# Optimization experiments

Measured on AMD Instinct MI355X. Metric: run time of the kernel, lower is better.

## Reference

```python
import jax, jax.numpy as jnp
import numpy as np

B, C, H, W = 8, 128, 128, 128
D_MODEL = C
D_INNER = 2 * D_MODEL          # expand=2 -> 256
D_STATE = 64
HEADDIM = 32                   # _resolve_headdim(128, 32) -> 32
NHEADS = D_INNER // HEADDIM    # 8
D_CONV = 4
CHUNK = 64
GN_GROUPS = 8                  # _group_count(128, 8)
D_XBC = D_INNER + 2 * D_STATE  # 384
D_INPROJ = 2 * D_INNER + 2 * D_STATE + NHEADS  # 648


def _group_norm(x, g, b, groups=GN_GROUPS, eps=1e-5):
    Bn, Cn, Hh, Ww = x.shape
    xr = x.reshape(Bn, groups, Cn // groups, Hh, Ww)
    mu = xr.mean(axis=(2, 3, 4), keepdims=True)
    var = xr.var(axis=(2, 3, 4), keepdims=True)
    xr = (xr - mu) * jax.lax.rsqrt(var + eps)
    return xr.reshape(Bn, Cn, Hh, Ww) * g[None, :, None, None] + b[None, :, None, None]


def _grid_sample_bilinear_border(img, grid):
    # img: (B,C,H,W); grid: (B,H,W,2) with (x,y) in [-1,1]; align_corners=True, border padding
    _, _, Hh, Ww = img.shape
    gx = jnp.clip((grid[..., 0] + 1.0) * 0.5 * (Ww - 1), 0.0, Ww - 1.0)
    gy = jnp.clip((grid[..., 1] + 1.0) * 0.5 * (Hh - 1), 0.0, Hh - 1.0)
    x0 = jnp.floor(gx); y0 = jnp.floor(gy)
    wx = gx - x0; wy = gy - y0
    x0i = x0.astype(jnp.int32); y0i = y0.astype(jnp.int32)
    x1i = jnp.minimum(x0i + 1, Ww - 1); y1i = jnp.minimum(y0i + 1, Hh - 1)
    def per_b(im, y0b, y1b, x0b, x1b, wxb, wyb):
        v00 = im[:, y0b, x0b]; v01 = im[:, y0b, x1b]
        v10 = im[:, y1b, x0b]; v11 = im[:, y1b, x1b]
        return (v00 * (1 - wxb) + v01 * wxb) * (1 - wyb) + (v10 * (1 - wxb) + v11 * wxb) * wyb
    return jax.vmap(per_b)(img, y0i, y1i, x0i, x1i, wx, wy)


def _mamba(seq, in_proj_w, conv_w, conv_b, dt_bias, A_log, D_skip, norm_g, out_w):
    # seq: (Bs, L, d_model) -> (Bs, L, d_model); Mamba2/SSD-style selective scan
    Bs, L, _ = seq.shape
    pad = (CHUNK - L % CHUNK) % CHUNK
    if pad:
        seq = jnp.pad(seq, ((0, 0), (0, pad), (0, 0)))
    Lp = L + pad
    zxbcdt = jnp.einsum('bld,ed->ble', seq, in_proj_w)
    z = zxbcdt[..., :D_INNER]
    xBC = zxbcdt[..., D_INNER:D_INNER + D_XBC]
    dt = jax.nn.softplus(zxbcdt[..., -NHEADS:] + dt_bias)  # (Bs,Lp,nh)
    # causal depthwise conv1d, kernel D_CONV
    xp = jnp.pad(xBC, ((0, 0), (D_CONV - 1, 0), (0, 0)))
    xBC = sum(conv_w[:, k] * xp[:, k:k + Lp, :] for k in range(D_CONV)) + conv_b
    xBC = jax.nn.silu(xBC)
    xs = xBC[..., :D_INNER].reshape(Bs, Lp, NHEADS, HEADDIM)
    Bm = xBC[..., D_INNER:D_INNER + D_STATE]
    Cm = xBC[..., D_INNER + D_STATE:]
    A = -jnp.exp(A_log)  # (nh,)
    def step(h, inp):
        x_t, B_t, C_t, dt_t = inp  # (Bs,nh,hd),(Bs,ds),(Bs,ds),(Bs,nh)
        dA = jnp.exp(dt_t * A)  # (Bs,nh)
        h = h * dA[..., None, None] + (dt_t[..., None] * x_t)[..., None] * B_t[:, None, None, :]
        y = jnp.einsum('bhds,bs->bhd', h, C_t)
        return h, y
    h0 = jnp.zeros((Bs, NHEADS, HEADDIM, D_STATE), seq.dtype)
    _, ys = jax.lax.scan(step, h0, (jnp.moveaxis(xs, 1, 0), jnp.moveaxis(Bm, 1, 0), jnp.moveaxis(Cm, 1, 0), jnp.moveaxis(dt, 1, 0)))
    ys = jnp.moveaxis(ys, 0, 1) + D_skip[None, None, :, None] * xs  # (Bs,Lp,nh,hd)
    y = ys.reshape(Bs, Lp, D_INNER) * jax.nn.silu(z)  # gated
    y = y * jax.lax.rsqrt(jnp.mean(y * y, axis=-1, keepdims=True) + 1e-5) * norm_g  # RMSNorm
    out = jnp.einsum('ble,de->bld', y, out_w)
    return out[:, :L] if pad else out


def _forward(x, dw_w, gn_g, gn_b, pw_w, pw_b, in_proj_w, conv_w, conv_b, dt_bias, A_log, D_skip, norm_g, out_w):
    Bn, Cn, Hh, Ww = x.shape
    dn = ('NCHW', 'OIHW', 'NCHW')
    # offset_net: depthwise 5x5 -> GroupNorm -> GELU -> 1x1
    h1 = jax.lax.conv_general_dilated(x, dw_w, (1, 1), 'SAME', feature_group_count=Cn, dimension_numbers=dn)
    h1 = jax.nn.gelu(_group_norm(h1, gn_g, gn_b), approximate=False)
    off = jax.lax.conv_general_dilated(h1, pw_w, (1, 1), 'SAME', dimension_numbers=dn) + pw_b[None, :, None, None]
    offset = jnp.tanh(off) * min(8.0, max(Hh, Ww) * 0.1)  # (B,1,H,W)
    gy = jnp.linspace(-1.0, 1.0, Hh, dtype=x.dtype)
    gx = jnp.linspace(-1.0, 1.0, Ww, dtype=x.dtype)
    base_y, base_x = jnp.meshgrid(gy, gx, indexing='ij')  # (H,W)
    off_n = offset[:, 0] * (2.0 / max(Hh - 1, 1))  # horizontal scan: vertical offsets
    grid = jnp.stack([jnp.broadcast_to(base_x, (Bn, Hh, Ww)), jnp.clip(base_y + off_n, -1.0, 1.0)], axis=-1)
    deformed = _grid_sample_bilinear_border(x, grid)
    seq = deformed.transpose(0, 2, 3, 1).reshape(Bn * Hh, Ww, Cn)  # (b h) w c
    out = _mamba(seq, in_proj_w, conv_w, conv_b, dt_bias, A_log, D_skip, norm_g, out_w)
    out_2d = out.reshape(Bn, Hh, Ww, Cn).transpose(0, 3, 1, 2)
    return out_2d, offset


def setup_inputs() -> dict:
    key = jax.random.key(0)
    ks = jax.random.split(key, 8)
    return {
        'x': jax.random.normal(ks[0], (B, C, H, W), jnp.float32),
        'dw_w': jax.random.normal(ks[1], (C, 1, 5, 5), jnp.float32) * 0.05,
        'gn_g': jnp.ones((C,), jnp.float32),
        'gn_b': jnp.zeros((C,), jnp.float32),
        'pw_w': jax.random.normal(ks[2], (1, C, 1, 1), jnp.float32) * 0.02,
        'pw_b': jnp.zeros((1,), jnp.float32),
        'in_proj_w': jax.random.normal(ks[3], (D_INPROJ, D_MODEL), jnp.float32) * 0.02,
        'conv_w': jax.random.normal(ks[4], (D_XBC, D_CONV), jnp.float32) * 0.1,
        'conv_b': jnp.zeros((D_XBC,), jnp.float32),
        'dt_bias': jax.random.normal(ks[5], (NHEADS,), jnp.float32) * 0.1,
        'A_log': jnp.log(jnp.arange(1, NHEADS + 1, dtype=jnp.float32)),
        'D_skip': jnp.ones((NHEADS,), jnp.float32),
        'norm_g': jnp.ones((D_INNER,), jnp.float32),
        'out_w': jax.random.normal(ks[6], (D_MODEL, D_INNER), jnp.float32) * 0.02,
    }


def reference(x, dw_w, gn_g, gn_b, pw_w, pw_b, in_proj_w, conv_w, conv_b, dt_bias, A_log, D_skip, norm_g, out_w):
    return _forward(x, dw_w, gn_g, gn_b, pw_w, pw_b, in_proj_w, conv_w, conv_b, dt_bias, A_log, D_skip, norm_g, out_w)
```

## Files before the change

kernel.cpp:

```cpp
#include <hip/hip_runtime.h>
#include <math.h>


typedef _Float16 half8 __attribute__((ext_vector_type(8)));
typedef _Float16 half4 __attribute__((ext_vector_type(4)));
typedef float f32x4 __attribute__((ext_vector_type(4)));

__device__ __forceinline__ float b2f(unsigned short u) {
  return __uint_as_float(((unsigned int)u) << 16);
}
__device__ __forceinline__ bool in_is_f32(const void* gng) {
  return ((const unsigned int*)gng)[0] == 0x3F800000u;
}

#define P_DWW 0
#define P_CW 3200
#define P_CB 4736
#define P_GNG 5120
#define P_GNB 5248
#define P_PWW 5376
#define P_PWB 5504
#define P_DTB 5505
#define P_ALOG 5513
#define P_DSKIP 5521
#define P_NG 5529

__global__ void k_prep_params(const void* dww, const void* cw, const void* cb,
                              const void* gng, const void* gnb, const void* pww,
                              const void* pwb, const void* dtbias, const void* alog,
                              const void* dskip, const void* ng, float* __restrict__ P,
                              float* __restrict__ gst) {
  bool f = in_is_f32(gng);
  int tid = threadIdx.x;
  if (tid < 128) gst[tid] = 0.f;
  auto cvt = [&](const void* src, int n, int off) {
    for (int i = tid; i < n; i += 256)
      P[off + i] = f ? ((const float*)src)[i] : b2f(((const unsigned short*)src)[i]);
  };
  cvt(dww, 3200, P_DWW);
  cvt(cw, 1536, P_CW);
  cvt(cb, 384, P_CB);
  cvt(gng, 128, P_GNG);
  cvt(gnb, 128, P_GNB);
  cvt(pww, 128, P_PWW);
  cvt(pwb, 1, P_PWB);
  cvt(dtbias, 8, P_DTB);
  cvt(alog, 8, P_ALOG);
  cvt(dskip, 8, P_DSKIP);
  cvt(ng, 256, P_NG);
}

__global__ void k_prep_w(const void* wproj, const void* outw, const void* gng,
                         _Float16* __restrict__ wprojh, _Float16* __restrict__ outwh) {
  bool f = in_is_f32(gng);
  int stride = gridDim.x * blockDim.x;
  for (int i = blockIdx.x * blockDim.x + threadIdx.x; i < 98304; i += stride) {
    int row = i >> 7;
    float v = 0.f;
    if (row < 648) v = f ? ((const float*)wproj)[i] : b2f(((const unsigned short*)wproj)[i]);
    wprojh[i] = (_Float16)v;
  }
  for (int i = blockIdx.x * blockDim.x + threadIdx.x; i < 32768; i += stride)
    outwh[i] = (_Float16)(f ? ((const float*)outw)[i] : b2f(((const unsigned short*)outw)[i]));
}

__global__ __launch_bounds__(256) void k_dwconv_v5(const void* __restrict__ x,
                                                   const void* __restrict__ gng,
                                                   const float* __restrict__ P,
                                                   _Float16* __restrict__ h1h,
                                                   float* __restrict__ gst) {
  int blk = blockIdx.x;
  int bc = blk >> 2, sub = blk & 3;
  int b = bc >> 7, c = bc & 127;
  int ty0 = sub * 32;
  bool f32x = in_is_f32(gng);
  __shared__ __align__(16) float t[36 * 136];
  __shared__ float red[8];
  const float* xf = (const float*)x + (size_t)bc * 16384;
  const unsigned short* xb = (const unsigned short*)x + (size_t)bc * 16384;
  for (int i = threadIdx.x; i < 72; i += 256) {
    int r = i >> 1;
    *(float4*)&t[136 * r + 128 + (i & 1) * 4] = make_float4(0.f, 0.f, 0.f, 0.f);
  }
  for (int i = threadIdx.x; i < 1152; i += 256) {
    int r = i >> 5, cq = i & 31;
    int gy = ty0 + r - 2;
    float4 v = make_float4(0.f, 0.f, 0.f, 0.f);
    if (gy >= 0 && gy < 128) {
      if (f32x) {
        v = *(const float4*)(xf + gy * 128 + cq * 4);
      } else {
        ushort4 u = *(const ushort4*)(xb + gy * 128 + cq * 4);
        v = make_float4(b2f(u.x), b2f(u.y), b2f(u.z), b2f(u.w));
      }
    }
    *(float4*)&t[136 * r + 4 * cq] = v;
  }
  float w[25];
#pragma unroll
  for (int k = 0; k < 25; ++k) w[k] = P[P_DWW + c * 25 + k];
  __syncthreads();

  int ox = (threadIdx.x & 31) * 4;
  int oy = (threadIdx.x >> 5) * 4;
  float acc[4][4];
#pragma unroll
  for (int r = 0; r < 4; ++r)
#pragma unroll
    for (int j = 0; j < 4; ++j) acc[r][j] = 0.f;

#pragma unroll
  for (int i = 0; i < 8; ++i) {
    int base = 136 * (oy + i);
    float4 c0 = make_float4(0.f, 0.f, 0.f, 0.f);
    if (ox >= 4) c0 = *(const float4*)&t[base + ox - 4];
    float4 c1 = *(const float4*)&t[base + ox];
    float4 c2 = *(const float4*)&t[base + ox + 4];
    float in12[12] = {c0.x, c0.y, c0.z, c0.w, c1.x, c1.y, c1.z, c1.w,
                      c2.x, c2.y, c2.z, c2.w};
#pragma unroll
    for (int r = 0; r < 4; ++r) {
      if (i - r >= 0 && i - r <= 4) {
        int ky = i - r;
#pragma unroll
        for (int j = 0; j < 4; ++j)
#pragma unroll
          for (int kx = 0; kx < 5; ++kx)
            acc[r][j] += w[ky * 5 + kx] * in12[j + kx + 2];
      }
    }
  }

  float s = 0.f, sq = 0.f;
  _Float16* hp = h1h + (size_t)bc * 16384;
#pragma unroll
  for (int r = 0; r < 4; ++r) {
    half4 o;
#pragma unroll
    for (int j = 0; j < 4; ++j) {
      o[j] = (_Float16)acc[r][j];
      s += acc[r][j]; sq += acc[r][j] * acc[r][j];
    }
    *(half4*)&hp[(ty0 + oy + r) * 128 + ox] = o;
  }
  for (int o = 32; o; o >>= 1) { s += __shfl_down(s, o, 64); sq += __shfl_down(sq, o, 64); }
  int wv = threadIdx.x >> 6;
  if ((threadIdx.x & 63) == 0) { red[wv] = s; red[4 + wv] = sq; }
  __syncthreads();
  if (threadIdx.x == 0) {
    float ts = red[0] + red[1] + red[2] + red[3];
    float tq = red[4] + red[5] + red[6] + red[7];
    int g = (b << 3) + (c >> 4);
    atomicAdd(&gst[g * 2], ts);
    atomicAdd(&gst[g * 2 + 1], tq);
  }
}

__global__ void k_stats(const float* __restrict__ gst, float* __restrict__ mr) {
  int g = threadIdx.x;
  if (g < 64) {
    const float invN = 1.f / 262144.f;
    float mean = gst[g * 2] * invN;
    float var = gst[g * 2 + 1] * invN - mean * mean;
    mr[g * 2] = mean;
    mr[g * 2 + 1] = rsqrtf(var + 1e-5f);
  }
}

__global__ __launch_bounds__(256) void k_gn_off_v3(const _Float16* __restrict__ h1h,
                                                   const float* __restrict__ mr,
                                                   const float* __restrict__ P,
                                                   float* __restrict__ offf,
                                                   float* __restrict__ dout) {
  int bh = blockIdx.x;
  int b = bh >> 7, h = bh & 127;
  int tid = threadIdx.x;
  int w = tid & 127;
  int chh = tid >> 7;
  __shared__ float sacc[2][128];
  float acc = 0.f;
  for (int ci = 0; ci < 64; ++ci) {
    int c = chh * 64 + ci;
    float v = (float)h1h[(((size_t)(b * 128 + c)) * 128 + h) * 128 + w];
    int g = b * 8 + (c >> 4);
    float nv = (v - mr[g * 2]) * mr[g * 2 + 1] * P[P_GNG + c] + P[P_GNB + c];
    float ge = 0.5f * nv * (1.f + erff(nv * 0.70710678118f));
    acc += ge * P[P_PWW + c];
  }
  sacc[chh][w] = acc;
  __syncthreads();
  if (chh == 0) {
    float off = acc + sacc[1][w] + P[P_PWB];
    float ofv = tanhf(off) * 8.0f;
    offf[bh * 128 + w] = ofv;
    dout[16777216 + bh * 128 + w] = ofv;
  }
}

__global__ __launch_bounds__(256) void k_deform_v3(const void* __restrict__ x,
                                                   const void* __restrict__ gng,
                                                   const float* __restrict__ offf,
                                                   _Float16* __restrict__ seqc,
                                                   int s0) {
  int bh = s0 + blockIdx.x;
  int b = bh >> 7, h = bh & 127;
  int tid = threadIdx.x;
  int w = tid & 127;
  int half = tid >> 7;
  bool f32x = in_is_f32(gng);
  __shared__ float t[128 * 129];
  float ofv = offf[bh * 128 + w];
  float gy = -1.f + (2.f / 127.f) * (float)h + ofv * (2.f / 127.f);
  gy = fminf(fmaxf(gy, -1.f), 1.f);
  float py = (gy + 1.f) * 0.5f * 127.f;
  py = fminf(fmaxf(py, 0.f), 127.f);
  float y0f = floorf(py);
  float wy = py - y0f;
  int y0 = (int)y0f;
  int y1 = min(y0 + 1, 127);
  const float* xfb = (const float*)x + (size_t)b * 128 * 16384;
  const unsigned short* xbb = (const unsigned short*)x + (size_t)b * 128 * 16384;
  int c0 = half * 64;
  for (int i = 0; i < 64; ++i) {
    int c = c0 + i;
    size_t o0 = (size_t)c * 16384 + y0 * 128 + w;
    size_t o1 = (size_t)c * 16384 + y1 * 128 + w;
    float v0, v1;
    if (f32x) { v0 = xfb[o0]; v1 = xfb[o1]; }
    else      { v0 = b2f(xbb[o0]); v1 = b2f(xbb[o1]); }
    t[c * 129 + w] = v0 + wy * (v1 - v0);
  }
  __syncthreads();
  int c2 = tid & 127;
  int lb = (tid >> 7) * 64;
  _Float16* sp = seqc + (size_t)blockIdx.x * 16384;
  for (int i = 0; i < 64; ++i) {
    int l = lb + i;
    sp[l * 128 + c2] = (_Float16)t[c2 * 129 + l];
  }
}

__global__ __launch_bounds__(256) void k_gemm1_v6(const _Float16* __restrict__ seqh,
                                                  const _Float16* __restrict__ wprojh,
                                                  const float* __restrict__ P,
                                                  _Float16* __restrict__ zh,
                                                  _Float16* __restrict__ xch,
                                                  float* __restrict__ dtb) {
  __shared__ __align__(16) _Float16 lds[16384];
  _Float16* lA = lds;
  _Float16* lB = lds + 8192;
  int m0 = blockIdx.x * 128;
  int e0 = blockIdx.y * 128;
  int tid = threadIdx.x;
  int lane = tid & 63;
  int wv = tid >> 6;
  f32x4 acc[2][8];
#pragma unroll
  for (int rf = 0; rf < 2; ++rf)
#pragma unroll
    for (int cf = 0; cf < 8; ++cf) acc[rf][cf] = (f32x4){0.f, 0.f, 0.f, 0.f};

  int rsel = lane & 15, q = lane >> 4;
  for (int k0 = 0; k0 < 128; k0 += 64) {
    if (k0) __syncthreads();
#pragma unroll
    for (int p = 0; p < 4; ++p) {
      int idx = tid + 256 * p;
      int row = idx >> 3, ch = idx & 7;
      int dch = ch ^ (row & 7);
      *(half8*)&lA[row * 64 + dch * 8] =
          *(const half8*)&seqh[(size_t)(m0 + row) * 128 + k0 + ch * 8];
      *(half8*)&lB[row * 64 + dch * 8] =
          *(const half8*)&wprojh[(size_t)(e0 + row) * 128 + k0 + ch * 8];
    }
    __syncthreads();
#pragma unroll
    for (int kk = 0; kk < 2; ++kk) {
      half8 a[2];
#pragma unroll
      for (int rf = 0; rf < 2; ++rf) {
        int row = wv * 32 + rf * 16 + rsel;
        int ch = (kk * 4 + q) ^ (row & 7);
        a[rf] = *(const half8*)&lA[row * 64 + ch * 8];
      }
#pragma unroll
      for (int cf = 0; cf < 8; ++cf) {
        int row = cf * 16 + rsel;
        int ch = (kk * 4 + q) ^ (row & 7);
        half8 b = *(const half8*)&lB[row * 64 + ch * 8];
        acc[0][cf] = __builtin_amdgcn_mfma_f32_16x16x32_f16(a[0], b, acc[0][cf], 0, 0, 0);
        acc[1][cf] = __builtin_amdgcn_mfma_f32_16x16x32_f16(a[1], b, acc[1][cf], 0, 0, 0);
      }
    }
  }

  if (e0 < 256) {
#pragma unroll
    for (int rf = 0; rf < 2; ++rf) {
      int mb = m0 + wv * 32 + rf * 16 + q * 4;
#pragma unroll
      for (int cf = 0; cf < 8; ++cf) {
        _Float16* pz = zh + (size_t)mb * 256 + e0 + cf * 16 + rsel;
#pragma unroll
        for (int r = 0; r < 4; ++r) pz[(size_t)r * 256] = (_Float16)acc[rf][cf][r];
      }
    }
  } else if (e0 < 640) {
    __syncthreads();
#pragma unroll
    for (int rf = 0; rf < 2; ++rf) {
#pragma unroll
      for (int r = 0; r < 4; ++r) {
        int row = wv * 32 + rf * 16 + q * 4 + r;
#pragma unroll
        for (int cf = 0; cf < 8; ++cf)
          lds[row * 128 + cf * 16 + rsel] = (_Float16)acc[rf][cf][r];
      }
    }
    __syncthreads();
    int cc = tid & 127;
    int rh = tid >> 7;
    int eg = (e0 - 256) + cc;
    float w0 = P[P_CW + eg * 4 + 0], w1 = P[P_CW + eg * 4 + 1];
    float w2 = P[P_CW + eg * 4 + 2], w3 = P[P_CW + eg * 4 + 3];
    float bb = P[P_CB + eg];
    int r0 = rh * 64;
    float x0 = (r0 >= 3) ? (float)lds[(r0 - 3) * 128 + cc] : 0.f;
    float x1 = (r0 >= 2) ? (float)lds[(r0 - 2) * 128 + cc] : 0.f;
    float x2 = (r0 >= 1) ? (float)lds[(r0 - 1) * 128 + cc] : 0.f;
    _Float16* xo = xch + (size_t)m0 * 384 + eg;
    for (int r = r0; r < r0 + 64; ++r) {
      float x3 = (float)lds[r * 128 + cc];
      float a = bb + w0 * x0 + w1 * x1 + w2 * x2 + w3 * x3;
      xo[(size_t)r * 384] = (_Float16)(a / (1.f + __expf(-a)));
      x0 = x1; x1 = x2; x2 = x3;
    }
  } else {
#pragma unroll
    for (int rf = 0; rf < 2; ++rf) {
      int mb = m0 + wv * 32 + rf * 16 + q * 4;
      if (rsel < 8) {
        float bias = P[P_DTB + rsel];
#pragma unroll
        for (int r = 0; r < 4; ++r) {
          float dv = acc[rf][0][r] + bias;
          float sp = (dv > 20.f) ? dv : log1pf(__expf(dv));
          dtb[(size_t)(mb + r) * 8 + rsel] = sp;
        }
      }
    }
  }
}

__global__ __launch_bounds__(256) void k_ssd(const _Float16* __restrict__ xch,
                                             const float* __restrict__ dtb,
                                             const float* __restrict__ P,
                                             _Float16* __restrict__ ys) {
  int seq = blockIdx.x;
  int tid = threadIdx.x;
  int lane = tid & 63, wv = tid >> 6;
  int rsel = lane & 15, q = lane >> 4;
  __shared__ __align__(16) _Float16 G[128 * 128];
  __shared__ __align__(16) _Float16 Xt[32 * 128];
  __shared__ float dts[128 * 8];
  __shared__ float Ts[8 * 128];
  const _Float16* xb = xch + (size_t)seq * 49152;
  const float* dtp = dtb + (size_t)seq * 1024;

  for (int i = tid; i < 1024; i += 256) dts[i] = dtp[i];
  __syncthreads();
  if (tid < 8) {
    float a = 0.f;
    for (int l = 0; l < 128; ++l) { a += dts[l * 8 + tid]; Ts[tid * 128 + l] = a; }
  }

  f32x4 gacc[2][8];
#pragma unroll
  for (int rf = 0; rf < 2; ++rf)
#pragma unroll
    for (int cf = 0; cf < 8; ++cf) gacc[rf][cf] = (f32x4){0.f, 0.f, 0.f, 0.f};
#pragma unroll
  for (int kk = 0; kk < 2; ++kk) {
    half8 a[2];
#pragma unroll
    for (int rf = 0; rf < 2; ++rf) {
      int l = wv * 32 + rf * 16 + rsel;
      a[rf] = *(const half8*)&xb[(size_t)l * 384 + 320 + kk * 32 + q * 8];
    }
#pragma unroll
    for (int cf = 0; cf < 8; ++cf) {
      int j = cf * 16 + rsel;
      half8 b = *(const half8*)&xb[(size_t)j * 384 + 256 + kk * 32 + q * 8];
      gacc[0][cf] = __builtin_amdgcn_mfma_f32_16x16x32_f16(a[0], b, gacc[0][cf], 0, 0, 0);
      gacc[1][cf] = __builtin_amdgcn_mfma_f32_16x16x32_f16(a[1], b, gacc[1][cf], 0, 0, 0);
    }
  }
#pragma unroll
  for (int rf = 0; rf < 2; ++rf) {
#pragma unroll
    for (int r = 0; r < 4; ++r) {
      int l = wv * 32 + rf * 16 + q * 4 + r;
#pragma unroll
      for (int cf = 0; cf < 8; ++cf) {
        int j = cf * 16 + rsel;
        G[l * 128 + (((j >> 3) ^ (l & 7)) << 3) + (j & 7)] = (_Float16)gacc[rf][cf][r];
      }
    }
  }
  __syncthreads();

  _Float16* yp = ys + (size_t)seq * 32768;
  for (int h = 0; h < 8; ++h) {
    {
      int j = tid >> 1, ds = (tid & 1) * 16;
      float dtj = dts[j * 8 + h];
      half8 v0 = *(const half8*)&xb[(size_t)j * 384 + h * 32 + ds];
      half8 v1 = *(const half8*)&xb[(size_t)j * 384 + h * 32 + ds + 8];
#pragma unroll
      for (int e = 0; e < 8; ++e) {
        int d0 = ds + e, d1 = ds + 8 + e;
        Xt[d0 * 128 + (((j >> 3) ^ (d0 & 7)) << 3) + (j & 7)] = (_Float16)((float)v0[e] * dtj);
        Xt[d1 * 128 + (((j >> 3) ^ (d1 & 7)) << 3) + (j & 7)] = (_Float16)((float)v1[e] * dtj);
      }
    }
    __syncthreads();
    float Ah = -__expf(P[P_ALOG + h]);
    float Dk = P[P_DSKIP + h];
    f32x4 acc[2][2];
#pragma unroll
    for (int rf = 0; rf < 2; ++rf)
#pragma unroll
      for (int cf = 0; cf < 2; ++cf) acc[rf][cf] = (f32x4){0.f, 0.f, 0.f, 0.f};
#pragma unroll
    for (int kk = 0; kk < 4; ++kk) {
      int jb = kk * 32 + q * 8;
      int chk = kk * 4 + q;
      float4 tj0 = *(const float4*)&Ts[h * 128 + jb];
      float4 tj1 = *(const float4*)&Ts[h * 128 + jb + 4];
      float tj[8] = {tj0.x, tj0.y, tj0.z, tj0.w, tj1.x, tj1.y, tj1.z, tj1.w};
      half8 a[2];
#pragma unroll
      for (int rf = 0; rf < 2; ++rf) {
        int l = wv * 32 + rf * 16 + rsel;
        half8 g = *(const half8*)&G[l * 128 + ((chk ^ (l & 7)) << 3)];
        float Tl = Ts[h * 128 + l];
        half8 w;
#pragma unroll
        for (int e = 0; e < 8; ++e) {
          int j = jb + e;
          float m = (j <= l) ? __expf(Ah * (Tl - tj[e])) : 0.f;
          w[e] = (_Float16)((float)g[e] * m);
        }
        a[rf] = w;
      }
#pragma unroll
      for (int cf = 0; cf < 2; ++cf) {
        int d = cf * 16 + rsel;
        half8 b = *(const half8*)&Xt[d * 128 + ((chk ^ (d & 7)) << 3)];
        acc[0][cf] = __builtin_amdgcn_mfma_f32_16x16x32_f16(a[0], b, acc[0][cf], 0, 0, 0);
        acc[1][cf] = __builtin_amdgcn_mfma_f32_16x16x32_f16(a[1], b, acc[1][cf], 0, 0, 0);
      }
    }
#pragma unroll
    for (int rf = 0; rf < 2; ++rf) {
      int lb = wv * 32 + rf * 16 + q * 4;
#pragma unroll
      for (int cf = 0; cf < 2; ++cf) {
        int d = cf * 16 + rsel;
#pragma unroll
        for (int r = 0; r < 4; ++r) {
          int l = lb + r;
          float xv = (float)xb[(size_t)l * 384 + h * 32 + d];
          yp[(size_t)l * 256 + h * 32 + d] = (_Float16)(acc[rf][cf][r] + Dk * xv);
        }
      }
    }
    __syncthreads();
  }
}

__global__ __launch_bounds__(256) void k_gate_v8(const _Float16* __restrict__ ys,
                                                 const _Float16* __restrict__ zh,
                                                 const float* __restrict__ P,
                                                 _Float16* __restrict__ ynh) {
  int seq = blockIdx.x;
  size_t base = (size_t)seq * 32768;
  int lane = threadIdx.x & 63;
  int wv = threadIdx.x >> 6;
  int sub = lane >> 5;
  int ln = lane & 31;
  for (int it = 0; it < 16; ++it) {
    int l = it * 8 + wv * 2 + sub;
    size_t off = base + (size_t)l * 256 + ln * 8;
    half8 yv8 = *(const half8*)&ys[off];
    half8 zv8 = *(const half8*)&zh[off];
    float yg[8];
    float ss = 0.f;
#pragma unroll
    for (int e = 0; e < 8; ++e) {
      float zv = (float)zv8[e];
      float g = zv / (1.f + __expf(-zv));
      float y = (float)yv8[e] * g;
      yg[e] = y;
      ss += y * y;
    }
    ss += __shfl_xor(ss, 1, 64);
    ss += __shfl_xor(ss, 2, 64);
    ss += __shfl_xor(ss, 4, 64);
    ss += __shfl_xor(ss, 8, 64);
    ss += __shfl_xor(ss, 16, 64);
    float r = rsqrtf(ss * (1.f / 256.f) + 1e-5f);
    half8 o;
#pragma unroll
    for (int e = 0; e < 8; ++e) o[e] = (_Float16)(yg[e] * r * P[P_NG + ln * 8 + e]);
    *(half8*)&ynh[off] = o;
  }
}

__global__ __launch_bounds__(256) void k_gemm2_v3(const _Float16* __restrict__ ynh,
                                                  const _Float16* __restrict__ outwh,
                                                  float* __restrict__ dout,
                                                  int tok0) {
  __shared__ __align__(16) _Float16 lA[128 * 64];
  __shared__ __align__(16) _Float16 lB[64 * 64];
  int t0 = blockIdx.x * 64;
  int tid = threadIdx.x;
  int lane = tid & 63;
  int wv = tid >> 6;
  f32x4 acc[2][4];
#pragma unroll
  for (int rf = 0; rf < 2; ++rf)
#pragma unroll
    for (int cf = 0; cf < 4; ++cf) acc[rf][cf] = (f32x4){0.f, 0.f, 0.f, 0.f};

  int rsel = lane & 15, q = lane >> 4;
  for (int k0 = 0; k0 < 256; k0 += 64) {
    if (k0) __syncthreads();
#pragma unroll
    for (int p = 0; p < 4; ++p) {
      int idx = tid + 256 * p;
      int row = idx >> 3, ch = idx & 7;
      int dch = ch ^ (row & 7);
      *(half8*)&lA[row * 64 + dch * 8] =
          *(const half8*)&outwh[(size_t)row * 256 + k0 + ch * 8];
    }
#pragma unroll
    for (int p = 0; p < 2; ++p) {
      int idx = tid + 256 * p;
      int row = idx >> 3, ch = idx & 7;
      int dch = ch ^ (row & 7);
      *(half8*)&lB[row * 64 + dch * 8] =
          *(const half8*)&ynh[(size_t)(t0 + row) * 256 + k0 + ch * 8];
    }
    __syncthreads();
#pragma unroll
    for (int kk = 0; kk < 2; ++kk) {
      half8 a[2];
#pragma unroll
      for (int rf = 0; rf < 2; ++rf) {
        int row = wv * 32 + rf * 16 + rsel;
        int ch = (kk * 4 + q) ^ (row & 7);
        a[rf] = *(const half8*)&lA[row * 64 + ch * 8];
      }
#pragma unroll
      for (int cf = 0; cf < 4; ++cf) {
        int row = cf * 16 + rsel;
        int ch = (kk * 4 + q) ^ (row & 7);
        half8 b = *(const half8*)&lB[row * 64 + ch * 8];
        acc[0][cf] = __builtin_amdgcn_mfma_f32_16x16x32_f16(a[0], b, acc[0][cf], 0, 0, 0);
        acc[1][cf] = __builtin_amdgcn_mfma_f32_16x16x32_f16(a[1], b, acc[1][cf], 0, 0, 0);
      }
    }
  }

  int l0 = tok0 + t0;
  int b = l0 >> 14;
  int rem0 = l0 & 16383;
#pragma unroll
  for (int rf = 0; rf < 2; ++rf) {
    int cbase = wv * 32 + rf * 16 + q * 4;
#pragma unroll
    for (int cf = 0; cf < 4; ++cf) {
#pragma unroll
      for (int r = 0; r < 4; ++r) {
        dout[(size_t)(b * 128 + cbase + r) * 16384 + rem0 + cf * 16 + rsel] = acc[rf][cf][r];
      }
    }
  }
}

extern "C" void kernel_launch(void* const* d_in, const int* in_sizes, int n_in,
                              void* d_out, int out_size, void* d_ws, size_t ws_size,
                              hipStream_t stream) {
  const void* x      = d_in[0];
  const void* dww    = d_in[1];
  const void* gng    = d_in[2];
  const void* gnb    = d_in[3];
  const void* pww    = d_in[4];
  const void* pwb    = d_in[5];
  const void* wproj  = d_in[6];
  const void* cw     = d_in[7];
  const void* cb     = d_in[8];
  const void* dtbias = d_in[9];
  const void* alog   = d_in[10];
  const void* dskip  = d_in[11];
  const void* ng     = d_in[12];
  const void* outw   = d_in[13];
  float* out = (float*)d_out;

  char* ws = (char*)d_ws;
  float* gst        = (float*)(ws + 0);
  float* mr         = (float*)(ws + 4096);
  float* P          = (float*)(ws + 8192);
  _Float16* wprojh  = (_Float16*)(ws + 40960);
  _Float16* outwh   = (_Float16*)(ws + 372736);
  float* offf       = (float*)(ws + 503808);
  char* cbase       = ws + 1028096;

  _Float16* h1h = (_Float16*)out;

  const int opts[11] = {1024, 512, 256, 128, 64, 32, 16, 8, 4, 2, 1};
  int CH = 1;
  for (int i = 0; i < 11; ++i) {
    if (1028096ull + (unsigned long long)opts[i] * 266240ull <= (unsigned long long)ws_size) {
      CH = opts[i];
      break;
    }
  }
  int NC = 1024 / CH;

  _Float16* seqh = (_Float16*)(cbase);
  _Float16* zh   = (_Float16*)(cbase + (size_t)CH * 32768);
  _Float16* xch  = (_Float16*)(cbase + (size_t)CH * 98304);
  float* dtbf    = (float*)(cbase + (size_t)CH * 196608);
  _Float16* ysh  = (_Float16*)(cbase + (size_t)CH * 200704);
  _Float16* ynh  = xch;

  k_prep_params<<<1, 256, 0, stream>>>(dww, cw, cb, gng, gnb, pww, pwb, dtbias,
                                       alog, dskip, ng, P, gst);
  k_prep_w<<<128, 256, 0, stream>>>(wproj, outw, gng, wprojh, outwh);
  k_dwconv_v5<<<4096, 256, 0, stream>>>(x, gng, P, h1h, gst);
  k_stats<<<1, 64, 0, stream>>>(gst, mr);
  k_gn_off_v3<<<1024, 256, 0, stream>>>(h1h, mr, P, offf, out);

  int M = CH * 128;
  for (int c = 0; c < NC; ++c) {
    int s0 = c * CH;
    k_deform_v3<<<CH, 256, 0, stream>>>(x, gng, offf, seqh, s0);
    k_gemm1_v6<<<dim3(M / 128, 6), 256, 0, stream>>>(seqh, wprojh, P, zh, xch, dtbf);
    k_ssd<<<CH, 256, 0, stream>>>(xch, dtbf, P, ysh);
    k_gate_v8<<<CH, 256, 0, stream>>>(ysh, zh, P, ynh);
    k_gemm2_v3<<<dim3(M / 64), 256, 0, stream>>>(ynh, outwh, out, s0 * 128);
  }
}
```

Baseline: 544.2 us.

## Merge prep kernels, fold GN stats into offset kernel, register-window depthwise conv

Result: slower. 599.7 us (+10.2%).

```diff
diff --git a/kernel.cpp b/kernel.cpp
--- a/kernel.cpp
+++ b/kernel.cpp
@@ -25,33 +25,13 @@
 #define P_DSKIP 5521
 #define P_NG 5529
 
-__global__ void k_prep_params(const void* dww, const void* cw, const void* cb,
-                              const void* gng, const void* gnb, const void* pww,
-                              const void* pwb, const void* dtbias, const void* alog,
-                              const void* dskip, const void* ng, float* __restrict__ P,
-                              float* __restrict__ gst) {
-  bool f = in_is_f32(gng);
-  int tid = threadIdx.x;
-  if (tid < 128) gst[tid] = 0.f;
-  auto cvt = [&](const void* src, int n, int off) {
-    for (int i = tid; i < n; i += 256)
-      P[off + i] = f ? ((const float*)src)[i] : b2f(((const unsigned short*)src)[i]);
-  };
-  cvt(dww, 3200, P_DWW);
-  cvt(cw, 1536, P_CW);
-  cvt(cb, 384, P_CB);
-  cvt(gng, 128, P_GNG);
-  cvt(gnb, 128, P_GNB);
-  cvt(pww, 128, P_PWW);
-  cvt(pwb, 1, P_PWB);
-  cvt(dtbias, 8, P_DTB);
-  cvt(alog, 8, P_ALOG);
-  cvt(dskip, 8, P_DSKIP);
-  cvt(ng, 256, P_NG);
-}
-
-__global__ void k_prep_w(const void* wproj, const void* outw, const void* gng,
-                         _Float16* __restrict__ wprojh, _Float16* __restrict__ outwh) {
+__global__ void k_prep_all(const void* dww, const void* cw, const void* cb,
+                           const void* gng, const void* gnb, const void* pww,
+                           const void* pwb, const void* dtbias, const void* alog,
+                           const void* dskip, const void* ng,
+                           const void* wproj, const void* outw,
+                           float* __restrict__ P, float* __restrict__ gst,
+                           _Float16* __restrict__ wprojh, _Float16* __restrict__ outwh) {
   bool f = in_is_f32(gng);
   int stride = gridDim.x * blockDim.x;
   for (int i = blockIdx.x * blockDim.x + threadIdx.x; i < 98304; i += stride) {
@@ -62,87 +42,105 @@
   }
   for (int i = blockIdx.x * blockDim.x + threadIdx.x; i < 32768; i += stride)
     outwh[i] = (_Float16)(f ? ((const float*)outw)[i] : b2f(((const unsigned short*)outw)[i]));
-}
-
-__global__ __launch_bounds__(256) void k_dwconv_v5(const void* __restrict__ x,
+  if (blockIdx.x == 0) {
+    int tid = threadIdx.x;
+    if (tid < 128) gst[tid] = 0.f;
+    auto cvt = [&](const void* src, int n, int off) {
+      for (int i = tid; i < n; i += 256)
+        P[off + i] = f ? ((const float*)src)[i] : b2f(((const unsigned short*)src)[i]);
+    };
+    cvt(dww, 3200, P_DWW);
+    cvt(cw, 1536, P_CW);
+    cvt(cb, 384, P_CB);
+    cvt(gng, 128, P_GNG);
+    cvt(gnb, 128, P_GNB);
+    cvt(pww, 128, P_PWW);
+    cvt(pwb, 1, P_PWB);
+    cvt(dtbias, 8, P_DTB);
+    cvt(alog, 8, P_ALOG);
+    cvt(dskip, 8, P_DSKIP);
+    cvt(ng, 256, P_NG);
+  }
+}
+
+__global__ __launch_bounds__(256) void k_dwconv_v6(const void* __restrict__ x,
                                                    const void* __restrict__ gng,
                                                    const float* __restrict__ P,
                                                    _Float16* __restrict__ h1h,
                                                    float* __restrict__ gst) {
-  int blk = blockIdx.x;
-  int bc = blk >> 2, sub = blk & 3;
+  int bc = blockIdx.x;
   int b = bc >> 7, c = bc & 127;
-  int ty0 = sub * 32;
   bool f32x = in_is_f32(gng);
-  __shared__ __align__(16) float t[36 * 136];
   __shared__ float red[8];
   const float* xf = (const float*)x + (size_t)bc * 16384;
   const unsigned short* xb = (const unsigned short*)x + (size_t)bc * 16384;
-  for (int i = threadIdx.x; i < 72; i += 256) {
-    int r = i >> 1;
-    *(float4*)&t[136 * r + 128 + (i & 1) * 4] = make_float4(0.f, 0.f, 0.f, 0.f);
-  }
-  for (int i = threadIdx.x; i < 1152; i += 256) {
-    int r = i >> 5, cq = i & 31;
-    int gy = ty0 + r - 2;
-    float4 v = make_float4(0.f, 0.f, 0.f, 0.f);
+  float w[25];
+#pragma unroll
+  for (int k = 0; k < 25; ++k) w[k] = P[P_DWW + c * 25 + k];
+
+  int ox = (threadIdx.x & 31) * 4;
+  int y0 = (threadIdx.x >> 5) * 16;
+  float win[5][12];
+
+  auto loadrow = [&](int gy, float* d) {
+#pragma unroll
+    for (int k = 0; k < 12; ++k) d[k] = 0.f;
     if (gy >= 0 && gy < 128) {
       if (f32x) {
-        v = *(const float4*)(xf + gy * 128 + cq * 4);
+        const float* rp = xf + gy * 128;
+        if (ox >= 4) {
+          float4 v = *(const float4*)(rp + ox - 4);
+          d[0] = v.x; d[1] = v.y; d[2] = v.z; d[3] = v.w;
+        }
+        float4 v0 = *(const float4*)(rp + ox);
+        d[4] = v0.x; d[5] = v0.y; d[6] = v0.z; d[7] = v0.w;
+        if (ox < 124) {
+          float4 v1 = *(const float4*)(rp + ox + 4);
+          d[8] = v1.x; d[9] = v1.y; d[10] = v1.z; d[11] = v1.w;
+        }
       } else {
-        ushort4 u = *(const ushort4*)(xb + gy * 128 + cq * 4);
-        v = make_float4(b2f(u.x), b2f(u.y), b2f(u.z), b2f(u.w));
-      }
-    }
-    *(float4*)&t[136 * r + 4 * cq] = v;
-  }
-  float w[25];
-#pragma unroll
-  for (int k = 0; k < 25; ++k) w[k] = P[P_DWW + c * 25 + k];
-  __syncthreads();
-
-  int ox = (threadIdx.x & 31) * 4;
-  int oy = (threadIdx.x >> 5) * 4;
-  float acc[4][4];
-#pragma unroll
-  for (int r = 0; r < 4; ++r)
-#pragma unroll
-    for (int j = 0; j < 4; ++j) acc[r][j] = 0.f;
-
-#pragma unroll
-  for (int i = 0; i < 8; ++i) {
-    int base = 136 * (oy + i);
-    float4 c0 = make_float4(0.f, 0.f, 0.f, 0.f);
-    if (ox >= 4) c0 = *(const float4*)&t[base + ox - 4];
-    float4 c1 = *(const float4*)&t[base + ox];
-    float4 c2 = *(const float4*)&t[base + ox + 4];
-    float in12[12] = {c0.x, c0.y, c0.z, c0.w, c1.x, c1.y, c1.z, c1.w,
-                      c2.x, c2.y, c2.z, c2.w};
-#pragma unroll
-    for (int r = 0; r < 4; ++r) {
-      if (i - r >= 0 && i - r <= 4) {
-        int ky = i - r;
-#pragma unroll
-        for (int j = 0; j < 4; ++j)
-#pragma unroll
-          for (int kx = 0; kx < 5; ++kx)
-            acc[r][j] += w[ky * 5 + kx] * in12[j + kx + 2];
-      }
-    }
-  }
+        const unsigned short* rp = xb + gy * 128;
+        if (ox >= 4) {
+          ushort4 u = *(const ushort4*)(rp + ox - 4);
+          d[0] = b2f(u.x); d[1] = b2f(u.y); d[2] = b2f(u.z); d[3] = b2f(u.w);
+        }
+        ushort4 u0 = *(const ushort4*)(rp + ox);
+        d[4] = b2f(u0.x); d[5] = b2f(u0.y); d[6] = b2f(u0.z); d[7] = b2f(u0.w);
+        if (ox < 124) {
+          ushort4 u1 = *(const ushort4*)(rp + ox + 4);
+          d[8] = b2f(u1.x); d[9] = b2f(u1.y); d[10] = b2f(u1.z); d[11] = b2f(u1.w);
+        }
+      }
+    }
+  };
+
+#pragma unroll
+  for (int i = 0; i < 4; ++i) loadrow(y0 - 2 + i, win[i]);
 
   float s = 0.f, sq = 0.f;
   _Float16* hp = h1h + (size_t)bc * 16384;
 #pragma unroll
-  for (int r = 0; r < 4; ++r) {
-    half4 o;
+  for (int yo = 0; yo < 16; ++yo) {
+    loadrow(y0 + yo + 2, win[(yo + 4) % 5]);
+    float o4[4] = {0.f, 0.f, 0.f, 0.f};
+#pragma unroll
+    for (int ky = 0; ky < 5; ++ky) {
+      const float* r = win[(yo + ky) % 5];
+#pragma unroll
+      for (int j = 0; j < 4; ++j)
+#pragma unroll
+        for (int kx = 0; kx < 5; ++kx)
+          o4[j] += w[ky * 5 + kx] * r[j + kx + 2];
+    }
+    half4 oh;
 #pragma unroll
     for (int j = 0; j < 4; ++j) {
-      o[j] = (_Float16)acc[r][j];
-      s += acc[r][j]; sq += acc[r][j] * acc[r][j];
-    }
-    *(half4*)&hp[(ty0 + oy + r) * 128 + ox] = o;
-  }
+      oh[j] = (_Float16)o4[j];
+      s += o4[j]; sq += o4[j] * o4[j];
+    }
+    *(half4*)&hp[(y0 + yo) * 128 + ox] = oh;
+  }
+
   for (int o = 32; o; o >>= 1) { s += __shfl_down(s, o, 64); sq += __shfl_down(sq, o, 64); }
   int wv = threadIdx.x >> 6;
   if ((threadIdx.x & 63) == 0) { red[wv] = s; red[4 + wv] = sq; }
@@ -156,19 +154,8 @@
   }
 }
 
-__global__ void k_stats(const float* __restrict__ gst, float* __restrict__ mr) {
-  int g = threadIdx.x;
-  if (g < 64) {
-    const float invN = 1.f / 262144.f;
-    float mean = gst[g * 2] * invN;
-    float var = gst[g * 2 + 1] * invN - mean * mean;
-    mr[g * 2] = mean;
-    mr[g * 2 + 1] = rsqrtf(var + 1e-5f);
-  }
-}
-
-__global__ __launch_bounds__(256) void k_gn_off_v3(const _Float16* __restrict__ h1h,
-                                                   const float* __restrict__ mr,
+__global__ __launch_bounds__(256) void k_gn_off_v4(const _Float16* __restrict__ h1h,
+                                                   const float* __restrict__ gst,
                                                    const float* __restrict__ P,
                                                    float* __restrict__ offf,
                                                    float* __restrict__ dout) {
@@ -178,14 +165,26 @@
   int w = tid & 127;
   int chh = tid >> 7;
   __shared__ float sacc[2][128];
+  const float invN = 1.f / 262144.f;
+  float gm[4], gr[4];
+#pragma unroll
+  for (int gg = 0; gg < 4; ++gg) {
+    int g = b * 8 + chh * 4 + gg;
+    float mean = gst[g * 2] * invN;
+    float var = gst[g * 2 + 1] * invN - mean * mean;
+    gm[gg] = mean;
+    gr[gg] = rsqrtf(var + 1e-5f);
+  }
   float acc = 0.f;
-  for (int ci = 0; ci < 64; ++ci) {
-    int c = chh * 64 + ci;
-    float v = (float)h1h[(((size_t)(b * 128 + c)) * 128 + h) * 128 + w];
-    int g = b * 8 + (c >> 4);
-    float nv = (v - mr[g * 2]) * mr[g * 2 + 1] * P[P_GNG + c] + P[P_GNB + c];
-    float ge = 0.5f * nv * (1.f + erff(nv * 0.70710678118f));
-    acc += ge * P[P_PWW + c];
+#pragma unroll
+  for (int gg = 0; gg < 4; ++gg) {
+    for (int ci = 0; ci < 16; ++ci) {
+      int c = chh * 64 + gg * 16 + ci;
+      float v = (float)h1h[(((size_t)(b * 128 + c)) * 128 + h) * 128 + w];
+      float nv = (v - gm[gg]) * gr[gg] * P[P_GNG + c] + P[P_GNB + c];
+      float ge = 0.5f * nv * (1.f + erff(nv * 0.70710678118f));
+      acc += ge * P[P_PWW + c];
+    }
   }
   sacc[chh][w] = acc;
   __syncthreads();
@@ -610,7 +609,6 @@
 
   char* ws = (char*)d_ws;
   float* gst        = (float*)(ws + 0);
-  float* mr         = (float*)(ws + 4096);
   float* P          = (float*)(ws + 8192);
   _Float16* wprojh  = (_Float16*)(ws + 40960);
   _Float16* outwh   = (_Float16*)(ws + 372736);
@@ -636,12 +634,11 @@
   _Float16* ysh  = (_Float16*)(cbase + (size_t)CH * 200704);
   _Float16* ynh  = xch;
 
-  k_prep_params<<<1, 256, 0, stream>>>(dww, cw, cb, gng, gnb, pww, pwb, dtbias,
-                                       alog, dskip, ng, P, gst);
-  k_prep_w<<<128, 256, 0, stream>>>(wproj, outw, gng, wprojh, outwh);
-  k_dwconv_v5<<<4096, 256, 0, stream>>>(x, gng, P, h1h, gst);
-  k_stats<<<1, 64, 0, stream>>>(gst, mr);
-  k_gn_off_v3<<<1024, 256, 0, stream>>>(h1h, mr, P, offf, out);
+  k_prep_all<<<128, 256, 0, stream>>>(dww, cw, cb, gng, gnb, pww, pwb, dtbias,
+                                      alog, dskip, ng, wproj, outw, P, gst,
+                                      wprojh, outwh);
+  k_dwconv_v6<<<1024, 256, 0, stream>>>(x, gng, P, h1h, gst);
+  k_gn_off_v4<<<1024, 256, 0, stream>>>(h1h, gst, P, offf, out);
 
   int M = CH * 128;
   for (int c = 0; c < NC; ++c) {
```
